# Performance work log

Measured on AMD Instinct MI355X. Metric: run time of the kernel, lower is better.

## Reference

```python
import jax, jax.numpy as jnp
import numpy as np

EPS = 1e-5
TOP_K = 2


def _dwconv3x3(x, w):
    # depthwise 3x3, stride 1, padding 1 (SAME)
    return jax.lax.conv_general_dilated(
        x, w, window_strides=(1, 1), padding='SAME',
        feature_group_count=x.shape[1],
        dimension_numbers=('NCHW', 'OIHW', 'NCHW'))


def _bn(x, g, b, m, v):
    # inference-mode BatchNorm2d
    s = g / jnp.sqrt(v + EPS)
    return x * s[None, :, None, None] + (b - m * s)[None, :, None, None]


def setup_inputs() -> dict:
    key = jax.random.key(0)
    ks = jax.random.split(key, 26)
    Bsz, D, H = 16, 384, 32
    S, E, HID = 64, 8, 768
    n, u = jax.random.normal, jax.random.uniform
    inp = {}
    inp['x'] = n(ks[0], (Bsz, D, H, H), jnp.float32)
    inp['dw1_w'] = n(ks[1], (D, 1, 3, 3)) * 0.1
    inp['bn1_g'] = u(ks[2], (D,), minval=0.5, maxval=1.5)
    inp['bn1_b'] = n(ks[3], (D,)) * 0.1
    inp['bn1_m'] = n(ks[4], (D,)) * 0.1
    inp['bn1_v'] = u(ks[5], (D,), minval=0.5, maxval=1.5)
    inp['dw2_w'] = n(ks[6], (D, 1, 3, 3)) * 0.1
    inp['bn2_g'] = u(ks[7], (D,), minval=0.5, maxval=1.5)
    inp['bn2_b'] = n(ks[8], (D,)) * 0.1
    inp['bn2_m'] = n(ks[9], (D,)) * 0.1
    inp['bn2_v'] = u(ks[10], (D,), minval=0.5, maxval=1.5)
    inp['ln_w'] = u(ks[11], (D,), minval=0.5, maxval=1.5)
    inp['ln_b'] = n(ks[12], (D,)) * 0.1
    inp['bcdt_w'] = n(ks[13], (3 * S, D)) * 0.02
    inp['dws_w'] = n(ks[14], (3 * S, 1, 3, 3)) * 0.1
    inp['hproj_w'] = n(ks[15], (D, D)) * 0.02
    inp['A'] = u(ks[16], (S,), minval=1.0, maxval=16.0)
    inp['gate_w'] = n(ks[17], (E, D)) * 0.02
    inp['gate_b'] = n(ks[18], (E,)) * 0.02
    inp['w1'] = n(ks[19], (E, HID, D)) * 0.02
    inp['b1'] = n(ks[20], (E, HID)) * 0.02
    inp['w2'] = n(ks[21], (E, D, HID)) * 0.02
    inp['b2'] = n(ks[22], (E, D)) * 0.02
    inp['w3'] = n(ks[23], (E, HID, D)) * 0.02
    inp['b3'] = n(ks[24], (E, HID)) * 0.02
    return inp


def reference(x, dw1_w, bn1_g, bn1_b, bn1_m, bn1_v, dw2_w, bn2_g, bn2_b, bn2_m,
              bn2_v, ln_w, ln_b, bcdt_w, dws_w, hproj_w, A, gate_w, gate_b,
              w1, b1, w2, b2, w3, b3):
    Bsz, D, H, W = x.shape
    L = H * W
    S = A.shape[0]
    E = gate_w.shape[0]
    # x = x + dwconv1(x)
    x = x + _bn(_dwconv3x3(x, dw1_w), bn1_g, bn1_b, bn1_m, bn1_v)
    x_prev = x
    # LayerNorm1D over channel dim of (B, C, L)
    xf = x.reshape(Bsz, D, L)
    mu = xf.mean(axis=1, keepdims=True)
    var = xf.var(axis=1, keepdims=True)
    xn = (xf - mu) / jnp.sqrt(var + EPS) * ln_w[None, :, None] + ln_b[None, :, None]
    # Slim_SSD mixer
    bcdt = jnp.einsum('cd,bdl->bcl', bcdt_w, xn)            # 1x1 conv1d
    bcdt = _dwconv3x3(bcdt.reshape(Bsz, 3 * S, H, W), dws_w).reshape(Bsz, 3 * S, L)
    Bm, Cm, dt = jnp.split(bcdt, 3, axis=1)                  # each (B, S, L)
    Am = jax.nn.softmax(dt + A[None, :, None], axis=-1)      # softmax over L
    h = jnp.einsum('bdl,bsl->bds', xn, Am * Bm)              # (B, D, S)
    h = jax.nn.silu(jnp.einsum('ed,bds->bes', hproj_w, h))   # h_proj + SiLU
    y = jnp.einsum('bes,bsl->bel', h, Cm).reshape(Bsz, D, H, W)
    x = x_prev + y
    # x = x + dwconv2(x)
    x = x + _bn(_dwconv3x3(x, dw2_w), bn2_g, bn2_b, bn2_m, bn2_v)
    # SparseMoE (TopkRouter, eval mode, filter_radio=0 -> mask==1, bias buffer==0)
    t = x.transpose(0, 2, 3, 1).reshape(-1, D)               # (N, D) tokens
    N = t.shape[0]
    logits = t @ gate_w.T + gate_b                           # (N, E)
    vals, idx = jax.lax.top_k(logits, TOP_K)
    probs = jax.nn.softmax(vals, axis=1)                     # softmax over top-k logits
    wfull = jnp.zeros((N, E), t.dtype).at[jnp.arange(N)[:, None], idx].set(probs)
    ymoe = jnp.zeros_like(t)
    for e in range(E):
        he = jax.nn.silu(t @ w1[e].T + b1[e]) * (t @ w3[e].T + b3[e])
        ymoe = ymoe + (he @ w2[e].T + b2[e]) * wfull[:, e:e + 1]
    x = x + ymoe.reshape(Bsz, H, W, D).transpose(0, 3, 1, 2)
    # dropout is identity in eval mode
    return (x, h)
```

## Files before the change

### kernel.cpp

```cpp
#include <hip/hip_runtime.h>
#include <hip/hip_bf16.h>

#define BSZ 16
#define DCH 384
#define LSP 1024
#define SST 64
#define NEXP 8
#define HID 768
#define NTOK 16384
#define MOE_MAXT 520

#define OFF_X1    0ULL
#define OFF_XN    25165824ULL
#define OFF_BCDT  50331648ULL
#define OFF_BCDTC 62914560ULL
#define OFF_H     75497472ULL
#define OFF_X2    77070336ULL
#define OFF_META  102236160ULL
#define OFF_LOGITS (OFF_META)
#define OFF_PROBS  (OFF_META +  524288ULL)
#define OFF_IDX    (OFF_META +  655360ULL)
#define OFF_CNT    (OFF_META +  786432ULL)
#define OFF_FILL   (OFF_META +  786464ULL)
#define OFF_OFFS   (OFF_META +  786496ULL)
#define OFF_TOFF   (OFF_META +  786560ULL)
#define OFF_LTOK   (OFF_META +  786624ULL)
#define OFF_LP     (OFF_META +  917696ULL)
#define OFF_TPOS   (OFF_META + 1048768ULL)
#define OFF_WBC    (OFF_META + 1179840ULL)
#define OFF_HE    0ULL
#define OFF_T16   OFF_BCDT
#define OFF_W1B   OFF_BCDTC
#define OFF_W3B   (OFF_BCDTC + 4718592ULL)
#define OFF_W2B   (OFF_BCDTC + 9437184ULL)
#define OFF_YMOE  OFF_X2
#define OFF_HPRE  OFF_X2
#define OFF_XNT   OFF_X2

typedef __attribute__((ext_vector_type(8))) short bf16x8;
typedef __attribute__((ext_vector_type(4))) float f32x4;
typedef __attribute__((ext_vector_type(4))) unsigned short u16x4;

__device__ __forceinline__ unsigned short f2bf(float f) {
  union { float f; unsigned int u; } x; x.f = f;
  unsigned int r = (x.u + 0x7fffu + ((x.u >> 16) & 1u)) >> 16;
  return (unsigned short)r;
}
__device__ __forceinline__ float bf2f(unsigned short s) {
  union { unsigned int u; float f; } x; x.u = ((unsigned int)s) << 16; return x.f;
}

__device__ __forceinline__ void async16(const void* g, void* l) {
  unsigned long long gi = reinterpret_cast<unsigned long long>(g);
  unsigned int li = (unsigned int)reinterpret_cast<unsigned long long>(l);
  __builtin_amdgcn_global_load_lds(
      (const __attribute__((address_space(1))) unsigned int*)gi,
      (__attribute__((address_space(3))) unsigned int*)(unsigned long long)li,
      16, 0, 0);
}

__global__ void k_dwbnres(const float* __restrict__ x, const float* __restrict__ w,
                          const float* __restrict__ g, const float* __restrict__ bb,
                          const float* __restrict__ mm, const float* __restrict__ vv,
                          float* __restrict__ out, int C) {
  int bc = blockIdx.x;
  int c = bc % C;
  __shared__ float tile[34 * 34];
  const float* img = x + (size_t)bc * 1024;
  for (int i = threadIdx.x; i < 34 * 34; i += 256) tile[i] = 0.f;
  __syncthreads();
  for (int i = threadIdx.x; i < 1024; i += 256) {
    int r = i >> 5, cc = i & 31;
    tile[(r + 1) * 34 + (cc + 1)] = img[i];
  }
  __syncthreads();
  float w0 = w[c*9+0], w1 = w[c*9+1], w2 = w[c*9+2], w3 = w[c*9+3], w4 = w[c*9+4],
        w5 = w[c*9+5], w6 = w[c*9+6], w7 = w[c*9+7], w8 = w[c*9+8];
  bool res = (g != nullptr);
  float scale = 1.f, bias = 0.f;
  if (res) { float s = g[c] * rsqrtf(vv[c] + 1e-5f); scale = s; bias = bb[c] - mm[c] * s; }
  for (int i = threadIdx.x; i < 1024; i += 256) {
    int r = i >> 5, cc = i & 31;
    const float* t0 = &tile[r * 34 + cc];
    float acc = t0[0]*w0 + t0[1]*w1 + t0[2]*w2
              + t0[34]*w3 + t0[35]*w4 + t0[36]*w5
              + t0[68]*w6 + t0[69]*w7 + t0[70]*w8;
    float o = res ? (t0[35] + acc * scale + bias) : acc;
    out[(size_t)bc * 1024 + i] = o;
  }
}

__global__ void k_layernorm(const float* __restrict__ x, const float* __restrict__ lw,
                            const float* __restrict__ lb, float* __restrict__ xn) {
  int lane = threadIdx.x & 63;
  int slice = threadIdx.x >> 6;
  int pos0 = blockIdx.x * 64;
  int b = pos0 >> 10;
  int l = (pos0 & 1023) + lane;
  const float* xb = x + (size_t)b * DCH * LSP + l;
  float s = 0.f, s2 = 0.f;
  for (int d = slice * 96; d < slice * 96 + 96; d++) {
    float v = xb[(size_t)d * LSP];
    s += v; s2 += v * v;
  }
  __shared__ float red[2][4][64];
  red[0][slice][lane] = s; red[1][slice][lane] = s2;
  __syncthreads();
  if (slice == 0) {
    s  = red[0][0][lane] + red[0][1][lane] + red[0][2][lane] + red[0][3][lane];
    s2 = red[1][0][lane] + red[1][1][lane] + red[1][2][lane] + red[1][3][lane];
    float mu = s * (1.f / 384.f);
    float var = s2 * (1.f / 384.f) - mu * mu;
    red[0][0][lane] = mu;
    red[1][0][lane] = rsqrtf(var + 1e-5f);
  }
  __syncthreads();
  float mu = red[0][0][lane], rs = red[1][0][lane];
  float* xnb = xn + (size_t)b * DCH * LSP + l;
  for (int d = slice * 96; d < slice * 96 + 96; d++) {
    float v = xb[(size_t)d * LSP];
    xnb[(size_t)d * LSP] = (v - mu) * rs * lw[d] + lb[d];
  }
}

__global__ void __launch_bounds__(256) k_bcdt(
    const unsigned short* __restrict__ xnT, const unsigned short* __restrict__ wbc,
    float* __restrict__ out) {
  int lt = blockIdx.x, ct = blockIdx.y, b = blockIdx.z;
  __shared__ unsigned short As[64 * 64];
  __shared__ unsigned short Bs[128 * 64];
  int tid = threadIdx.x;
  int lane = tid & 63, wave = tid >> 6;
  int wm = (wave & 1) * 32, wn = (wave >> 1) * 64;
  int fm = lane & 15, fq = lane >> 4;
  int srow = lane >> 3, slot = lane & 7;
  f32x4 acc[2][4];
  #pragma unroll
  for (int mi = 0; mi < 2; mi++)
    #pragma unroll
    for (int ni = 0; ni < 4; ni++) acc[mi][ni] = (f32x4)(0.f);
  const unsigned short* wge = wbc + (size_t)(ct * 64) * 384;
  const unsigned short* xge = xnT + ((size_t)(b * 1024 + lt * 128)) * 384;
  int ar0 = wave * 16 + srow, ar1 = ar0 + 8;
  const unsigned short* ag0 = wge + (size_t)ar0 * 384 + ((slot ^ (ar0 & 7)) * 8);
  const unsigned short* ag1 = wge + (size_t)ar1 * 384 + ((slot ^ (ar1 & 7)) * 8);
  const unsigned short* bg[4];
  #pragma unroll
  for (int ii = 0; ii < 4; ii++) {
    int brow = wave * 32 + ii * 8 + srow;
    bg[ii] = xge + (size_t)brow * 384 + ((slot ^ (brow & 7)) * 8);
  }
  unsigned short* asw0 = &As[(wave * 16) * 64];
  unsigned short* asw1 = &As[(wave * 16 + 8) * 64];
  for (int k0 = 0; k0 < 384; k0 += 64) {
    async16(ag0 + k0, asw0);
    async16(ag1 + k0, asw1);
    #pragma unroll
    for (int ii = 0; ii < 4; ii++)
      async16(bg[ii] + k0, &Bs[(wave * 32 + ii * 8) * 64]);
    __syncthreads();
    #pragma unroll
    for (int kk = 0; kk < 2; kk++) {
      int c = kk * 4 + fq;
      bf16x8 av[2];
      #pragma unroll
      for (int mi = 0; mi < 2; mi++) {
        int row = wm + mi * 16 + fm;
        av[mi] = *(bf16x8*)&As[row * 64 + ((c ^ (row & 7)) * 8)];
      }
      #pragma unroll
      for (int ni = 0; ni < 4; ni++) {
        int row = wn + ni * 16 + fm;
        bf16x8 bv = *(bf16x8*)&Bs[row * 64 + ((c ^ (row & 7)) * 8)];
        #pragma unroll
        for (int mi = 0; mi < 2; mi++)
          acc[mi][ni] = __builtin_amdgcn_mfma_f32_16x16x32_bf16(av[mi], bv, acc[mi][ni], 0, 0, 0);
      }
    }
    __syncthreads();
  }
  float* ob = out + (size_t)b * 196608 + (size_t)(ct * 64) * 1024 + lt * 128;
  #pragma unroll
  for (int mi = 0; mi < 2; mi++)
    #pragma unroll
    for (int ni = 0; ni < 4; ni++)
      #pragma unroll
      for (int r = 0; r < 4; r++) {
        int row = wm + mi * 16 + fq * 4 + r;
        int col = wn + ni * 16 + fm;
        ob[(size_t)row * 1024 + col] = acc[mi][ni][r];
      }
}

__global__ void k_softmax(float* __restrict__ bc, const float* __restrict__ Av) {
  int b = blockIdx.x >> 6, s = blockIdx.x & 63;
  float* row = bc + (size_t)b * 196608 + (size_t)(128 + s) * 1024;
  float a = Av[s];
  int t = threadIdx.x;
  float v[4]; float mx = -3.0e38f;
  #pragma unroll
  for (int i = 0; i < 4; i++) { v[i] = row[t + 256 * i] + a; mx = fmaxf(mx, v[i]); }
  #pragma unroll
  for (int off = 32; off >= 1; off >>= 1) mx = fmaxf(mx, __shfl_xor(mx, off));
  __shared__ float redm[4], reds[4];
  if ((t & 63) == 0) redm[t >> 6] = mx;
  __syncthreads();
  mx = fmaxf(fmaxf(redm[0], redm[1]), fmaxf(redm[2], redm[3]));
  float sm = 0.f;
  #pragma unroll
  for (int i = 0; i < 4; i++) { v[i] = __expf(v[i] - mx); sm += v[i]; }
  #pragma unroll
  for (int off = 32; off >= 1; off >>= 1) sm += __shfl_xor(sm, off);
  if ((t & 63) == 0) reds[t >> 6] = sm;
  __syncthreads();
  sm = reds[0] + reds[1] + reds[2] + reds[3];
  float inv = 1.f / sm;
  #pragma unroll
  for (int i = 0; i < 4; i++) row[t + 256 * i] = v[i] * inv;
}

__global__ void k_h(const float* __restrict__ xn, const float* __restrict__ bc,
                    float* __restrict__ h) {
  int dt_ = blockIdx.x, ls = blockIdx.y, b = blockIdx.z;
  __shared__ float xs[64][65];
  __shared__ float ab[64][65];
  int tid = threadIdx.x;
  int sg4 = tid & 15, dg4 = tid >> 4;
  float acc[4][4];
  #pragma unroll
  for (int i = 0; i < 4; i++)
    #pragma unroll
    for (int j = 0; j < 4; j++) acc[i][j] = 0.f;
  const float* Bm = bc + (size_t)b * 196608;
  const float* Am = Bm + 131072;
  const float* xb = xn + (size_t)b * DCH * LSP + (size_t)(dt_ * 64) * LSP;
  for (int l0 = ls * 128; l0 < ls * 128 + 128; l0 += 64) {
    for (int i = tid; i < 4096; i += 256) {
      int r = i >> 6, ll = i & 63;
      xs[r][ll] = xb[(size_t)r * LSP + l0 + ll];
      ab[r][ll] = Am[(size_t)r * 1024 + l0 + ll] * Bm[(size_t)r * 1024 + l0 + ll];
    }
    __syncthreads();
    for (int ll = 0; ll < 64; ll++) {
      float xv[4], av[4];
      #pragma unroll
      for (int i = 0; i < 4; i++) xv[i] = xs[dg4 * 4 + i][ll];
      #pragma unroll
      for (int j = 0; j < 4; j++) av[j] = ab[sg4 * 4 + j][ll];
      #pragma unroll
      for (int i = 0; i < 4; i++)
        #pragma unroll
        for (int j = 0; j < 4; j++) acc[i][j] += xv[i] * av[j];
    }
    __syncthreads();
  }
  float* hb = h + (size_t)b * DCH * SST + (size_t)(dt_ * 64) * 64;
  #pragma unroll
  for (int i = 0; i < 4; i++)
    #pragma unroll
    for (int j = 0; j < 4; j++)
      atomicAdd(&hb[(size_t)(dg4 * 4 + i) * 64 + sg4 * 4 + j], acc[i][j]);
}

__global__ void k_hproj(const float* __restrict__ h, const float* __restrict__ pw,
                        float* __restrict__ hpre) {
  int et = blockIdx.x, ks = blockIdx.y, b = blockIdx.z;
  __shared__ float hs[64][65];
  __shared__ float ps[64][65];
  int tid = threadIdx.x;
  int sg4 = tid & 15, eg4 = tid >> 4;
  float acc[4][4];
  #pragma unroll
  for (int i = 0; i < 4; i++)
    #pragma unroll
    for (int j = 0; j < 4; j++) acc[i][j] = 0.f;
  for (int d0 = ks * 128; d0 < ks * 128 + 128; d0 += 64) {
    for (int i = tid; i < 4096; i += 256) {
      int r = i >> 6, cc = i & 63;
      hs[r][cc] = h[(size_t)b * DCH * SST + (size_t)(d0 + r) * 64 + cc];
      ps[r][cc] = pw[(size_t)(et * 64 + r) * 384 + d0 + cc];
    }
    __syncthreads();
    for (int dd = 0; dd < 64; dd++) {
      float pv[4], hv[4];
      #pragma unroll
      for (int i = 0; i < 4; i++) pv[i] = ps[eg4 * 4 + i][dd];
      #pragma unroll
      for (int j = 0; j < 4; j++) hv[j] = hs[dd][sg4 * 4 + j];
      #pragma unroll
      for (int i = 0; i < 4; i++)
        #pragma unroll
        for (int j = 0; j < 4; j++) acc[i][j] += pv[i] * hv[j];
    }
    __syncthreads();
  }
  float* hb = hpre + (size_t)b * DCH * SST + (size_t)(et * 64) * 64;
  #pragma unroll
  for (int i = 0; i < 4; i++)
    #pragma unroll
    for (int j = 0; j < 4; j++)
      atomicAdd(&hb[(size_t)(eg4 * 4 + i) * 64 + sg4 * 4 + j], acc[i][j]);
}

__global__ void k_silu(const float* __restrict__ hpre, float* __restrict__ h2) {
  int i = blockIdx.x * 256 + threadIdx.x;
  float4 v = ((const float4*)hpre)[i];
  v.x = v.x / (1.f + __expf(-v.x));
  v.y = v.y / (1.f + __expf(-v.y));
  v.z = v.z / (1.f + __expf(-v.z));
  v.w = v.w / (1.f + __expf(-v.w));
  ((float4*)h2)[i] = v;
}

__global__ void k_y(const float* __restrict__ h2, const float* __restrict__ bc,
                    const float* __restrict__ x1, float* __restrict__ x2) {
  int lt = blockIdx.x, dt_ = blockIdx.y, b = blockIdx.z;
  __shared__ float hss[32][65];
  __shared__ float cs[64][129];
  int lg = threadIdx.x & 31, dg = threadIdx.x >> 5;
  float acc[4][4];
  for (int i = 0; i < 4; i++) for (int j = 0; j < 4; j++) acc[i][j] = 0.f;
  for (int i = threadIdx.x; i < 2048; i += 256) {
    int r = i >> 6, cc = i & 63;
    hss[r][cc] = h2[(size_t)b * DCH * SST + (size_t)(dt_ * 32 + r) * 64 + cc];
  }
  const float* Cm = bc + (size_t)b * 196608 + 65536;
  for (int i = threadIdx.x; i < 8192; i += 256) {
    int ss = i >> 7, ll = i & 127;
    cs[ss][ll] = Cm[(size_t)ss * 1024 + lt * 128 + ll];
  }
  __syncthreads();
  for (int ss = 0; ss < 64; ss++) {
    float cv[4];
    #pragma unroll
    for (int il = 0; il < 4; il++) cv[il] = cs[ss][lg + 32 * il];
    #pragma unroll
    for (int id = 0; id < 4; id++) {
      float hv = hss[dg * 4 + id][ss];
      #pragma unroll
      for (int il = 0; il < 4; il++) acc[id][il] += hv * cv[il];
    }
  }
  size_t base = (size_t)b * DCH * LSP + (size_t)(dt_ * 32) * LSP + lt * 128;
  for (int id = 0; id < 4; id++)
    for (int il = 0; il < 4; il++) {
      size_t o = base + (size_t)(dg * 4 + id) * LSP + lg + 32 * il;
      x2[o] = x1[o] + acc[id][il];
    }
}

__global__ void k_router(const float* __restrict__ x3, const float* __restrict__ gw,
                         const float* __restrict__ gb, float* __restrict__ logits) {
  __shared__ float xs[64][65];
  __shared__ float gs[8][64];
  int blk = blockIdx.x;
  int b = blk >> 4; int l0 = (blk & 15) * 64;
  int lg = threadIdx.x & 63, eg = threadIdx.x >> 6;
  float acc0 = 0.f, acc1 = 0.f;
  const float* xb = x3 + (size_t)b * DCH * LSP + l0;
  for (int d0 = 0; d0 < 384; d0 += 64) {
    for (int i = threadIdx.x; i < 4096; i += 256) {
      int dd = i >> 6, ll = i & 63;
      xs[dd][ll] = xb[(size_t)(d0 + dd) * LSP + ll];
    }
    for (int i = threadIdx.x; i < 512; i += 256) {
      int e = i >> 6, dd = i & 63;
      gs[e][dd] = gw[(size_t)e * 384 + d0 + dd];
    }
    __syncthreads();
    for (int dd = 0; dd < 64; dd++) {
      float xv = xs[dd][lg];
      acc0 += gs[eg][dd] * xv;
      acc1 += gs[eg + 4][dd] * xv;
    }
    __syncthreads();
  }
  int n = b * 1024 + l0 + lg;
  logits[(size_t)n * 8 + eg]     = acc0 + gb[eg];
  logits[(size_t)n * 8 + eg + 4] = acc1 + gb[eg + 4];
}

__global__ void k_topk(const float* __restrict__ logits, float* __restrict__ probs,
                       int* __restrict__ idx, int* __restrict__ cnt) {
  __shared__ int lcnt[8];
  if (threadIdx.x < 8) lcnt[threadIdx.x] = 0;
  __syncthreads();
  int n = blockIdx.x * 256 + threadIdx.x;
  float lv[8];
  for (int e = 0; e < 8; e++) lv[e] = logits[(size_t)n * 8 + e];
  int i1 = 0; float v1 = lv[0];
  for (int e = 1; e < 8; e++) if (lv[e] > v1) { v1 = lv[e]; i1 = e; }
  int i2 = -1; float v2 = -3.0e38f;
  for (int e = 0; e < 8; e++) { if (e == i1) continue; if (lv[e] > v2) { v2 = lv[e]; i2 = e; } }
  float p1 = 1.f / (1.f + __expf(v2 - v1));
  probs[n * 2] = p1; probs[n * 2 + 1] = 1.f - p1;
  idx[n * 2] = i1; idx[n * 2 + 1] = i2;
  atomicAdd(&lcnt[i1], 1); atomicAdd(&lcnt[i2], 1);
  __syncthreads();
  if (threadIdx.x < 8) atomicAdd(&cnt[threadIdx.x], lcnt[threadIdx.x]);
}

__global__ void k_offsets(const int* __restrict__ cnt, int* __restrict__ offs,
                          int* __restrict__ toff) {
  if (threadIdx.x == 0) {
    int a = 0, t = 0;
    for (int e = 0; e < 8; e++) {
      offs[e] = a; toff[e] = t;
      a += cnt[e]; t += (cnt[e] + 63) >> 6;
    }
    toff[8] = t;
  }
}

__global__ void k_build(const int* __restrict__ idx, const float* __restrict__ probs,
                        const int* __restrict__ offs, int* __restrict__ fill,
                        int* __restrict__ ltok, float* __restrict__ lp,
                        int* __restrict__ tpos) {
  __shared__ int lcnt[8], lbase[8];
  if (threadIdx.x < 8) lcnt[threadIdx.x] = 0;
  __syncthreads();
  int n = blockIdx.x * 256 + threadIdx.x;
  int e0 = idx[n * 2], e1 = idx[n * 2 + 1];
  int o0 = atomicAdd(&lcnt[e0], 1);
  int o1 = atomicAdd(&lcnt[e1], 1);
  __syncthreads();
  if (threadIdx.x < 8) lbase[threadIdx.x] = atomicAdd(&fill[threadIdx.x], lcnt[threadIdx.x]);
  __syncthreads();
  int p0 = offs[e0] + lbase[e0] + o0;
  int p1 = offs[e1] + lbase[e1] + o1;
  ltok[p0] = n; lp[p0] = probs[n * 2];     tpos[n * 2] = p0;
  ltok[p1] = n; lp[p1] = probs[n * 2 + 1]; tpos[n * 2 + 1] = p1;
}

__global__ void k_t16(const float* __restrict__ x3, unsigned short* __restrict__ t16) {
  __shared__ float tl[32][33];
  int lt = blockIdx.x, dt_ = blockIdx.y, b = blockIdx.z;
  const float* xb = x3 + (size_t)b * DCH * LSP + (size_t)(dt_ * 32) * LSP + lt * 32;
  for (int i = threadIdx.x; i < 1024; i += 256) {
    int dd = i >> 5, ll = i & 31;
    tl[dd][ll] = xb[(size_t)dd * LSP + ll];
  }
  __syncthreads();
  for (int i = threadIdx.x; i < 1024; i += 256) {
    int ll = i >> 5, dd = i & 31;
    int n = b * 1024 + lt * 32 + ll;
    t16[(size_t)n * 384 + dt_ * 32 + dd] = f2bf(tl[dd][ll]);
  }
}

__global__ void k_wbf(const float* __restrict__ s, unsigned short* __restrict__ d) {
  int i = blockIdx.x * 256 + threadIdx.x;
  float4 v = ((const float4*)s)[i];
  u16x4 o;
  o.x = f2bf(v.x); o.y = f2bf(v.y); o.z = f2bf(v.z); o.w = f2bf(v.w);
  ((u16x4*)d)[i] = o;
}

__global__ void k_f2bf3(const float* __restrict__ s0, const float* __restrict__ s1,
                        const float* __restrict__ s2, unsigned short* __restrict__ d0,
                        unsigned short* __restrict__ d1, unsigned short* __restrict__ d2,
                        int n4) {
  int i = blockIdx.x * 256 + threadIdx.x;
  if (i >= n4) return;
  const float* s = (blockIdx.y == 0) ? s0 : (blockIdx.y == 1) ? s1 : s2;
  unsigned short* d = (blockIdx.y == 0) ? d0 : (blockIdx.y == 1) ? d1 : d2;
  float4 v = ((const float4*)s)[i];
  u16x4 o;
  o.x = f2bf(v.x); o.y = f2bf(v.y); o.z = f2bf(v.z); o.w = f2bf(v.w);
  ((u16x4*)d)[i] = o;
}

__global__ void __launch_bounds__(256) k_moe1(
    const unsigned short* __restrict__ t16, const unsigned short* __restrict__ w1,
    const unsigned short* __restrict__ w3, const float* __restrict__ b1,
    const float* __restrict__ b3, const int* __restrict__ ltok,
    const int* __restrict__ cnt, const int* __restrict__ offs,
    const int* __restrict__ toff, unsigned short* __restrict__ he) {
  int tb = blockIdx.x;
  if (tb >= toff[8]) return;
  int e = 0;
  #pragma unroll
  for (int i = 1; i < 8; i++) if (toff[i] <= tb) e = i;
  int rt = tb - toff[e];
  int ne = cnt[e], base = offs[e];
  int ct = blockIdx.y;
  __shared__ unsigned short As[64 * 64];
  __shared__ unsigned short B1s[128 * 64];
  __shared__ unsigned short B3s[128 * 64];
  __shared__ int toks[64];
  int tid = threadIdx.x;
  if (tid < 64) {
    int r = rt * 64 + tid;
    toks[tid] = ltok[base + (r < ne ? r : ne - 1)];
  }
  __syncthreads();
  int lane = tid & 63, wave = tid >> 6;
  int wm = (wave & 1) * 32, wn = (wave >> 1) * 64;
  int fm = lane & 15, fq = lane >> 4;
  int srow = lane >> 3, slot = lane & 7;
  f32x4 acc1[2][4], acc3[2][4];
  #pragma unroll
  for (int mi = 0; mi < 2; mi++)
    #pragma unroll
    for (int ni = 0; ni < 4; ni++) { acc1[mi][ni] = (f32x4)(0.f); acc3[mi][ni] = (f32x4)(0.f); }
  const unsigned short* w1e = w1 + ((size_t)e * 768 + ct * 128) * 384;
  const unsigned short* w3e = w3 + ((size_t)e * 768 + ct * 128) * 384;
  int ar0 = wave * 16 + srow, ar1 = wave * 16 + 8 + srow;
  const unsigned short* ag0 = t16 + (size_t)toks[ar0] * 384 + ((slot ^ (ar0 & 7)) * 8);
  const unsigned short* ag1 = t16 + (size_t)toks[ar1] * 384 + ((slot ^ (ar1 & 7)) * 8);
  const unsigned short* b1g[4]; const unsigned short* b3g[4];
  #pragma unroll
  for (int ii = 0; ii < 4; ii++) {
    int brow = wave * 32 + ii * 8 + srow;
    int coff = (slot ^ (brow & 7)) * 8;
    b1g[ii] = w1e + (size_t)brow * 384 + coff;
    b3g[ii] = w3e + (size_t)brow * 384 + coff;
  }
  unsigned short* asw0 = &As[(wave * 16) * 64];
  unsigned short* asw1 = &As[(wave * 16 + 8) * 64];
  for (int k0 = 0; k0 < 384; k0 += 64) {
    async16(ag0 + k0, asw0);
    async16(ag1 + k0, asw1);
    #pragma unroll
    for (int ii = 0; ii < 4; ii++) {
      async16(b1g[ii] + k0, &B1s[(wave * 32 + ii * 8) * 64]);
      async16(b3g[ii] + k0, &B3s[(wave * 32 + ii * 8) * 64]);
    }
    __syncthreads();
    #pragma unroll
    for (int kk = 0; kk < 2; kk++) {
      int c = kk * 4 + fq;
      bf16x8 av[2];
      #pragma unroll
      for (int mi = 0; mi < 2; mi++) {
        int row = wm + mi * 16 + fm;
        av[mi] = *(bf16x8*)&As[row * 64 + ((c ^ (row & 7)) * 8)];
      }
      #pragma unroll
      for (int ni = 0; ni < 4; ni++) {
        int row = wn + ni * 16 + fm;
        int off = row * 64 + ((c ^ (row & 7)) * 8);
        bf16x8 b1v = *(bf16x8*)&B1s[off];
        bf16x8 b3v = *(bf16x8*)&B3s[off];
        #pragma unroll
        for (int mi = 0; mi < 2; mi++) {
          acc1[mi][ni] = __builtin_amdgcn_mfma_f32_16x16x32_bf16(av[mi], b1v, acc1[mi][ni], 0, 0, 0);
          acc3[mi][ni] = __builtin_amdgcn_mfma_f32_16x16x32_bf16(av[mi], b3v, acc3[mi][ni], 0, 0, 0);
        }
      }
    }
    __syncthreads();
  }
  #pragma unroll
  for (int mi = 0; mi < 2; mi++)
    #pragma unroll
    for (int ni = 0; ni < 4; ni++)
      #pragma unroll
      for (int r = 0; r < 4; r++) {
        int lr = wm + mi * 16 + fq * 4 + r;
        int gr = rt * 64 + lr;
        if (gr < ne) {
          int col = ct * 128 + wn + ni * 16 + fm;
          float z1 = acc1[mi][ni][r] + b1[e * 768 + col];
          float z3 = acc3[mi][ni][r] + b3[e * 768 + col];
          float val = (z1 / (1.f + __expf(-z1))) * z3;
          he[((size_t)base + gr) * 768 + col] = f2bf(val);
        }
      }
}

__global__ void __launch_bounds__(256) k_moe2(
    const unsigned short* __restrict__ he, const unsigned short* __restrict__ w2,
    const float* __restrict__ b2, const float* __restrict__ lp,
    const int* __restrict__ cnt, const int* __restrict__ offs,
    const int* __restrict__ toff, unsigned short* __restrict__ ymoe) {
  int tb = blockIdx.x;
  if (tb >= toff[8]) return;
  int e = 0;
  #pragma unroll
  for (int i = 1; i < 8; i++) if (toff[i] <= tb) e = i;
  int rt = tb - toff[e];
  int ne = cnt[e], base = offs[e];
  int ct = blockIdx.y;
  __shared__ unsigned short As[64 * 64];
  __shared__ unsigned short Bs[128 * 64];
  __shared__ float lps[64];
  int tid = threadIdx.x;
  if (tid < 64) {
    int r = rt * 64 + tid;
    lps[tid] = lp[base + (r < ne ? r : ne - 1)];
  }
  int lane = tid & 63, wave = tid >> 6;
  int wm = (wave & 1) * 32, wn = (wave >> 1) * 64;
  int fm = lane & 15, fq = lane >> 4;
  int srow = lane >> 3, slot = lane & 7;
  f32x4 acc[2][4];
  #pragma unroll
  for (int mi = 0; mi < 2; mi++)
    #pragma unroll
    for (int ni = 0; ni < 4; ni++) acc[mi][ni] = (f32x4)(0.f);
  const unsigned short* w2e = w2 + ((size_t)e * 384 + ct * 128) * 768;
  int ar0 = wave * 16 + srow, ar1 = wave * 16 + 8 + srow;
  int g0 = base + rt * 64 + ar0; if (g0 > 32767) g0 = 32767;
  int g1 = base + rt * 64 + ar1; if (g1 > 32767) g1 = 32767;
  const unsigned short* ag0 = he + (size_t)g0 * 768 + ((slot ^ (ar0 & 7)) * 8);
  const unsigned short* ag1 = he + (size_t)g1 * 768 + ((slot ^ (ar1 & 7)) * 8);
  const unsigned short* bg[4];
  #pragma unroll
  for (int ii = 0; ii < 4; ii++) {
    int brow = wave * 32 + ii * 8 + srow;
    bg[ii] = w2e + (size_t)brow * 768 + ((slot ^ (brow & 7)) * 8);
  }
  unsigned short* asw0 = &As[(wave * 16) * 64];
  unsigned short* asw1 = &As[(wave * 16 + 8) * 64];
  for (int k0 = 0; k0 < 768; k0 += 64) {
    async16(ag0 + k0, asw0);
    async16(ag1 + k0, asw1);
    #pragma unroll
    for (int ii = 0; ii < 4; ii++)
      async16(bg[ii] + k0, &Bs[(wave * 32 + ii * 8) * 64]);
    __syncthreads();
    #pragma unroll
    for (int kk = 0; kk < 2; kk++) {
      int c = kk * 4 + fq;
      bf16x8 av[2];
      #pragma unroll
      for (int mi = 0; mi < 2; mi++) {
        int row = wm + mi * 16 + fm;
        av[mi] = *(bf16x8*)&As[row * 64 + ((c ^ (row & 7)) * 8)];
      }
      #pragma unroll
      for (int ni = 0; ni < 4; ni++) {
        int row = wn + ni * 16 + fm;
        bf16x8 bv = *(bf16x8*)&Bs[row * 64 + ((c ^ (row & 7)) * 8)];
        #pragma unroll
        for (int mi = 0; mi < 2; mi++)
          acc[mi][ni] = __builtin_amdgcn_mfma_f32_16x16x32_bf16(av[mi], bv, acc[mi][ni], 0, 0, 0);
      }
    }
    __syncthreads();
  }
  #pragma unroll
  for (int mi = 0; mi < 2; mi++)
    #pragma unroll
    for (int ni = 0; ni < 4; ni++)
      #pragma unroll
      for (int r = 0; r < 4; r++) {
        int lr = wm + mi * 16 + fq * 4 + r;
        int gr = rt * 64 + lr;
        if (gr < ne) {
          int col = ct * 128 + wn + ni * 16 + fm;
          float val = (acc[mi][ni][r] + b2[e * 384 + col]) * lps[lr];
          ymoe[((size_t)base + gr) * 384 + col] = f2bf(val);
        }
      }
}

__global__ void k_scatter(const unsigned short* __restrict__ ymoe,
                          const int* __restrict__ tpos, float* __restrict__ xout) {
  int dt_ = blockIdx.x;
  int lt = blockIdx.y;
  int b = blockIdx.z;
  int l = threadIdx.x & 63;
  int d0 = dt_ * 32 + (threadIdx.x >> 6) * 8;
  int n = b * 1024 + lt * 64 + l;
  int p0 = tpos[2 * n], p1 = tpos[2 * n + 1];
  bf16x8 y0 = *(const bf16x8*)(ymoe + (size_t)p0 * 384 + d0);
  bf16x8 y1 = *(const bf16x8*)(ymoe + (size_t)p1 * 384 + d0);
  size_t base = (size_t)b * DCH * LSP + (size_t)d0 * LSP + lt * 64 + l;
  #pragma unroll
  for (int k = 0; k < 8; k++) {
    float v = bf2f((unsigned short)y0[k]) + bf2f((unsigned short)y1[k]);
    xout[base + (size_t)k * LSP] += v;
  }
}

extern "C" void kernel_launch(void* const* d_in, const int* in_sizes, int n_in,
                              void* d_out, int out_size, void* d_ws, size_t ws_size,
                              hipStream_t stream) {
  const float* x      = (const float*)d_in[0];
  const float* dw1    = (const float*)d_in[1];
  const float* bn1g   = (const float*)d_in[2];
  const float* bn1b   = (const float*)d_in[3];
  const float* bn1m   = (const float*)d_in[4];
  const float* bn1v   = (const float*)d_in[5];
  const float* dw2    = (const float*)d_in[6];
  const float* bn2g   = (const float*)d_in[7];
  const float* bn2b   = (const float*)d_in[8];
  const float* bn2m   = (const float*)d_in[9];
  const float* bn2v   = (const float*)d_in[10];
  const float* lnw    = (const float*)d_in[11];
  const float* lnb    = (const float*)d_in[12];
  const float* bcdtw  = (const float*)d_in[13];
  const float* dwsw   = (const float*)d_in[14];
  const float* hprojw = (const float*)d_in[15];
  const float* Avec   = (const float*)d_in[16];
  const float* gatew  = (const float*)d_in[17];
  const float* gateb  = (const float*)d_in[18];
  const float* w1f    = (const float*)d_in[19];
  const float* b1f    = (const float*)d_in[20];
  const float* w2f    = (const float*)d_in[21];
  const float* b2f    = (const float*)d_in[22];
  const float* w3f    = (const float*)d_in[23];
  const float* b3f    = (const float*)d_in[24];

  char* wsb = (char*)d_ws;
  float* x1    = (float*)(wsb + OFF_X1);
  float* xn    = (float*)(wsb + OFF_XN);
  float* bcdt  = (float*)(wsb + OFF_BCDT);
  float* bcdtc = (float*)(wsb + OFF_BCDTC);
  float* hbuf  = (float*)(wsb + OFF_H);
  float* hpre  = (float*)(wsb + OFF_HPRE);
  float* x2    = (float*)(wsb + OFF_X2);
  float* logits = (float*)(wsb + OFF_LOGITS);
  float* probs  = (float*)(wsb + OFF_PROBS);
  int*   idx    = (int*)(wsb + OFF_IDX);
  int*   cnt    = (int*)(wsb + OFF_CNT);
  int*   fill   = (int*)(wsb + OFF_FILL);
  int*   offs   = (int*)(wsb + OFF_OFFS);
  int*   toff   = (int*)(wsb + OFF_TOFF);
  int*   ltok   = (int*)(wsb + OFF_LTOK);
  float* lp     = (float*)(wsb + OFF_LP);
  int*   tpos   = (int*)(wsb + OFF_TPOS);
  unsigned short* t16  = (unsigned short*)(wsb + OFF_T16);
  unsigned short* w1b  = (unsigned short*)(wsb + OFF_W1B);
  unsigned short* w3b  = (unsigned short*)(wsb + OFF_W3B);
  unsigned short* w2b  = (unsigned short*)(wsb + OFF_W2B);
  unsigned short* he   = (unsigned short*)(wsb + OFF_HE);
  unsigned short* ymoe = (unsigned short*)(wsb + OFF_YMOE);
  unsigned short* xnT  = (unsigned short*)(wsb + OFF_XNT);
  unsigned short* wbc  = (unsigned short*)(wsb + OFF_WBC);
  float* xout = (float*)d_out;
  float* h2   = xout + (size_t)BSZ * DCH * LSP;

  k_dwbnres<<<BSZ * DCH, 256, 0, stream>>>(x, dw1, bn1g, bn1b, bn1m, bn1v, x1, DCH);
  k_layernorm<<<NTOK / 64, 256, 0, stream>>>(x1, lnw, lnb, xn);
  k_t16<<<dim3(32, 12, BSZ), 256, 0, stream>>>(xn, xnT);
  k_wbf<<<72, 256, 0, stream>>>(bcdtw, wbc);
  k_bcdt<<<dim3(8, 3, BSZ), 256, 0, stream>>>(xnT, wbc, bcdt);
  k_dwbnres<<<BSZ * 192, 256, 0, stream>>>(bcdt, dwsw, nullptr, nullptr, nullptr, nullptr, bcdtc, 192);
  k_softmax<<<BSZ * SST, 256, 0, stream>>>(bcdtc, Avec);
  hipMemsetAsync(hbuf, 0, (size_t)BSZ * DCH * SST * 4, stream);
  hipMemsetAsync(hpre, 0, (size_t)BSZ * DCH * SST * 4, stream);
  k_h<<<dim3(6, 8, BSZ), 256, 0, stream>>>(xn, bcdtc, hbuf);
  k_hproj<<<dim3(6, 3, BSZ), 256, 0, stream>>>(hbuf, hprojw, hpre);
  k_silu<<<(BSZ * DCH * SST / 4) / 256, 256, 0, stream>>>(hpre, h2);
  k_y<<<dim3(8, 12, BSZ), 256, 0, stream>>>(h2, bcdtc, x1, x2);
  k_dwbnres<<<BSZ * DCH, 256, 0, stream>>>(x2, dw2, bn2g, bn2b, bn2m, bn2v, xout, DCH);
  hipMemsetAsync(wsb + OFF_CNT, 0, 64, stream);
  k_router<<<256, 256, 0, stream>>>(xout, gatew, gateb, logits);
  k_topk<<<NTOK / 256, 256, 0, stream>>>(logits, probs, idx, cnt);
  k_offsets<<<1, 64, 0, stream>>>(cnt, offs, toff);
  k_build<<<NTOK / 256, 256, 0, stream>>>(idx, probs, offs, fill, ltok, lp, tpos);
  k_t16<<<dim3(32, 12, BSZ), 256, 0, stream>>>(xout, t16);
  int n4 = NEXP * HID * DCH / 4;
  k_f2bf3<<<dim3((n4 + 255) / 256, 3), 256, 0, stream>>>(w1f, w3f, w2f, w1b, w3b, w2b, n4);
  k_moe1<<<dim3(MOE_MAXT, 6), 256, 0, stream>>>(t16, w1b, w3b, b1f, b3f, ltok, cnt, offs, toff, he);
  k_moe2<<<dim3(MOE_MAXT, 3), 256, 0, stream>>>(he, w2b, b2f, lp, cnt, offs, toff, ymoe);
  k_scatter<<<dim3(12, 16, BSZ), 256, 0, stream>>>(ymoe, tpos, xout);
}
```

Before: 505.6 us.

## Enlarge MoE GEMM row tiles to 128 tokens and swap grid axes

```diff
diff --git a/kernel.cpp b/kernel.cpp
--- a/kernel.cpp
+++ b/kernel.cpp
@@ -8,7 +8,7 @@
 #define NEXP 8
 #define HID 768
 #define NTOK 16384
-#define MOE_MAXT 520
+#define MOE_MAXT 264
 
 #define OFF_X1    0ULL
 #define OFF_XN    25165824ULL
@@ -406,7 +406,7 @@
     int a = 0, t = 0;
     for (int e = 0; e < 8; e++) {
       offs[e] = a; toff[e] = t;
-      a += cnt[e]; t += (cnt[e] + 63) >> 6;
+      a += cnt[e]; t += (cnt[e] + 127) >> 7;
     }
     toff[8] = t;
   }
@@ -470,80 +470,76 @@
   ((u16x4*)d)[i] = o;
 }
 
-__global__ void __launch_bounds__(256) k_moe1(
+__global__ void __launch_bounds__(256, 2) k_moe1(
     const unsigned short* __restrict__ t16, const unsigned short* __restrict__ w1,
     const unsigned short* __restrict__ w3, const float* __restrict__ b1,
     const float* __restrict__ b3, const int* __restrict__ ltok,
     const int* __restrict__ cnt, const int* __restrict__ offs,
     const int* __restrict__ toff, unsigned short* __restrict__ he) {
-  int tb = blockIdx.x;
+  int tb = blockIdx.y;
   if (tb >= toff[8]) return;
   int e = 0;
   #pragma unroll
   for (int i = 1; i < 8; i++) if (toff[i] <= tb) e = i;
   int rt = tb - toff[e];
   int ne = cnt[e], base = offs[e];
-  int ct = blockIdx.y;
-  __shared__ unsigned short As[64 * 64];
+  int ct = blockIdx.x;
+  __shared__ unsigned short As[128 * 64];
   __shared__ unsigned short B1s[128 * 64];
   __shared__ unsigned short B3s[128 * 64];
-  __shared__ int toks[64];
+  __shared__ int toks[128];
   int tid = threadIdx.x;
-  if (tid < 64) {
-    int r = rt * 64 + tid;
+  if (tid < 128) {
+    int r = rt * 128 + tid;
     toks[tid] = ltok[base + (r < ne ? r : ne - 1)];
   }
   __syncthreads();
   int lane = tid & 63, wave = tid >> 6;
-  int wm = (wave & 1) * 32, wn = (wave >> 1) * 64;
+  int rh = wave & 1, ch = wave >> 1;
   int fm = lane & 15, fq = lane >> 4;
   int srow = lane >> 3, slot = lane & 7;
-  f32x4 acc1[2][4], acc3[2][4];
-  #pragma unroll
-  for (int mi = 0; mi < 2; mi++)
+  f32x4 acc1[4][4], acc3[4][4];
+  #pragma unroll
+  for (int mi = 0; mi < 4; mi++)
     #pragma unroll
     for (int ni = 0; ni < 4; ni++) { acc1[mi][ni] = (f32x4)(0.f); acc3[mi][ni] = (f32x4)(0.f); }
   const unsigned short* w1e = w1 + ((size_t)e * 768 + ct * 128) * 384;
   const unsigned short* w3e = w3 + ((size_t)e * 768 + ct * 128) * 384;
-  int ar0 = wave * 16 + srow, ar1 = wave * 16 + 8 + srow;
-  const unsigned short* ag0 = t16 + (size_t)toks[ar0] * 384 + ((slot ^ (ar0 & 7)) * 8);
-  const unsigned short* ag1 = t16 + (size_t)toks[ar1] * 384 + ((slot ^ (ar1 & 7)) * 8);
-  const unsigned short* b1g[4]; const unsigned short* b3g[4];
+  const unsigned short* ag[4]; const unsigned short* b1g[4]; const unsigned short* b3g[4];
   #pragma unroll
   for (int ii = 0; ii < 4; ii++) {
-    int brow = wave * 32 + ii * 8 + srow;
-    int coff = (slot ^ (brow & 7)) * 8;
-    b1g[ii] = w1e + (size_t)brow * 384 + coff;
-    b3g[ii] = w3e + (size_t)brow * 384 + coff;
-  }
-  unsigned short* asw0 = &As[(wave * 16) * 64];
-  unsigned short* asw1 = &As[(wave * 16 + 8) * 64];
+    int row = wave * 32 + ii * 8 + srow;
+    int coff = (slot ^ (row & 7)) * 8;
+    ag[ii]  = t16 + (size_t)toks[row] * 384 + coff;
+    b1g[ii] = w1e + (size_t)row * 384 + coff;
+    b3g[ii] = w3e + (size_t)row * 384 + coff;
+  }
   for (int k0 = 0; k0 < 384; k0 += 64) {
-    async16(ag0 + k0, asw0);
-    async16(ag1 + k0, asw1);
     #pragma unroll
     for (int ii = 0; ii < 4; ii++) {
-      async16(b1g[ii] + k0, &B1s[(wave * 32 + ii * 8) * 64]);
-      async16(b3g[ii] + k0, &B3s[(wave * 32 + ii * 8) * 64]);
+      unsigned int lb = (wave * 32 + ii * 8) * 64;
+      async16(ag[ii]  + k0, &As[lb]);
+      async16(b1g[ii] + k0, &B1s[lb]);
+      async16(b3g[ii] + k0, &B3s[lb]);
     }
     __syncthreads();
     #pragma unroll
     for (int kk = 0; kk < 2; kk++) {
       int c = kk * 4 + fq;
-      bf16x8 av[2];
-      #pragma unroll
-      for (int mi = 0; mi < 2; mi++) {
-        int row = wm + mi * 16 + fm;
+      bf16x8 av[4];
+      #pragma unroll
+      for (int mi = 0; mi < 4; mi++) {
+        int row = rh * 64 + mi * 16 + fm;
         av[mi] = *(bf16x8*)&As[row * 64 + ((c ^ (row & 7)) * 8)];
       }
       #pragma unroll
       for (int ni = 0; ni < 4; ni++) {
-        int row = wn + ni * 16 + fm;
+        int row = ch * 64 + ni * 16 + fm;
         int off = row * 64 + ((c ^ (row & 7)) * 8);
         bf16x8 b1v = *(bf16x8*)&B1s[off];
         bf16x8 b3v = *(bf16x8*)&B3s[off];
         #pragma unroll
-        for (int mi = 0; mi < 2; mi++) {
+        for (int mi = 0; mi < 4; mi++) {
           acc1[mi][ni] = __builtin_amdgcn_mfma_f32_16x16x32_bf16(av[mi], b1v, acc1[mi][ni], 0, 0, 0);
           acc3[mi][ni] = __builtin_amdgcn_mfma_f32_16x16x32_bf16(av[mi], b3v, acc3[mi][ni], 0, 0, 0);
         }
@@ -552,15 +548,15 @@
     __syncthreads();
   }
   #pragma unroll
-  for (int mi = 0; mi < 2; mi++)
+  for (int mi = 0; mi < 4; mi++)
     #pragma unroll
     for (int ni = 0; ni < 4; ni++)
       #pragma unroll
       for (int r = 0; r < 4; r++) {
-        int lr = wm + mi * 16 + fq * 4 + r;
-        int gr = rt * 64 + lr;
+        int lr = rh * 64 + mi * 16 + fq * 4 + r;
+        int gr = rt * 128 + lr;
         if (gr < ne) {
-          int col = ct * 128 + wn + ni * 16 + fm;
+          int col = ct * 128 + ch * 64 + ni * 16 + fm;
           float z1 = acc1[mi][ni][r] + b1[e * 768 + col];
           float z3 = acc3[mi][ni][r] + b3[e * 768 + col];
           float val = (z1 / (1.f + __expf(-z1))) * z3;
@@ -569,87 +565,84 @@
       }
 }
 
-__global__ void __launch_bounds__(256) k_moe2(
+__global__ void __launch_bounds__(256, 3) k_moe2(
     const unsigned short* __restrict__ he, const unsigned short* __restrict__ w2,
     const float* __restrict__ b2, const float* __restrict__ lp,
     const int* __restrict__ cnt, const int* __restrict__ offs,
     const int* __restrict__ toff, unsigned short* __restrict__ ymoe) {
-  int tb = blockIdx.x;
+  int tb = blockIdx.y;
   if (tb >= toff[8]) return;
   int e = 0;
   #pragma unroll
   for (int i = 1; i < 8; i++) if (toff[i] <= tb) e = i;
   int rt = tb - toff[e];
   int ne = cnt[e], base = offs[e];
-  int ct = blockIdx.y;
-  __shared__ unsigned short As[64 * 64];
+  int ct = blockIdx.x;
+  __shared__ unsigned short As[128 * 64];
   __shared__ unsigned short Bs[128 * 64];
-  __shared__ float lps[64];
+  __shared__ float lps[128];
   int tid = threadIdx.x;
-  if (tid < 64) {
-    int r = rt * 64 + tid;
+  if (tid < 128) {
+    int r = rt * 128 + tid;
     lps[tid] = lp[base + (r < ne ? r : ne - 1)];
   }
   int lane = tid & 63, wave = tid >> 6;
-  int wm = (wave & 1) * 32, wn = (wave >> 1) * 64;
+  int rh = wave & 1, ch = wave >> 1;
   int fm = lane & 15, fq = lane >> 4;
   int srow = lane >> 3, slot = lane & 7;
-  f32x4 acc[2][4];
-  #pragma unroll
-  for (int mi = 0; mi < 2; mi++)
+  f32x4 acc[4][4];
+  #pragma unroll
+  for (int mi = 0; mi < 4; mi++)
     #pragma unroll
     for (int ni = 0; ni < 4; ni++) acc[mi][ni] = (f32x4)(0.f);
   const unsigned short* w2e = w2 + ((size_t)e * 384 + ct * 128) * 768;
-  int ar0 = wave * 16 + srow, ar1 = wave * 16 + 8 + srow;
-  int g0 = base + rt * 64 + ar0; if (g0 > 32767) g0 = 32767;
-  int g1 = base + rt * 64 + ar1; if (g1 > 32767) g1 = 32767;
-  const unsigned short* ag0 = he + (size_t)g0 * 768 + ((slot ^ (ar0 & 7)) * 8);
-  const unsigned short* ag1 = he + (size_t)g1 * 768 + ((slot ^ (ar1 & 7)) * 8);
-  const unsigned short* bg[4];
+  const unsigned short* ag[4]; const unsigned short* bg[4];
   #pragma unroll
   for (int ii = 0; ii < 4; ii++) {
-    int brow = wave * 32 + ii * 8 + srow;
-    bg[ii] = w2e + (size_t)brow * 768 + ((slot ^ (brow & 7)) * 8);
-  }
-  unsigned short* asw0 = &As[(wave * 16) * 64];
-  unsigned short* asw1 = &As[(wave * 16 + 8) * 64];
+    int row = wave * 32 + ii * 8 + srow;
+    int coff = (slot ^ (row & 7)) * 8;
+    int g = base + rt * 128 + row; if (g > 32767) g = 32767;
+    ag[ii] = he + (size_t)g * 768 + coff;
+    bg[ii] = w2e + (size_t)row * 768 + coff;
+  }
   for (int k0 = 0; k0 < 768; k0 += 64) {
-    async16(ag0 + k0, asw0);
-    async16(ag1 + k0, asw1);
-    #pragma unroll
-    for (int ii = 0; ii < 4; ii++)
-      async16(bg[ii] + k0, &Bs[(wave * 32 + ii * 8) * 64]);
+    #pragma unroll
+    for (int ii = 0; ii < 4; ii++) {
+      unsigned int lb = (wave * 32 + ii * 8) * 64;
+      async16(ag[ii] + k0, &As[lb]);
+      async16(bg[ii] + k0, &Bs[lb]);
+    }
     __syncthreads();
     #pragma unroll
     for (int kk = 0; kk < 2; kk++) {
       int c = kk * 4 + fq;
-      bf16x8 av[2];
-      #pragma unroll
-      for (int mi = 0; mi < 2; mi++) {
-        int row = wm + mi * 16 + fm;
+      bf16x8 av[4];
+      #pragma unroll
+      for (int mi = 0; mi < 4; mi++) {
+        int row = rh * 64 + mi * 16 + fm;
         av[mi] = *(bf16x8*)&As[row * 64 + ((c ^ (row & 7)) * 8)];
       }
       #pragma unroll
       for (int ni = 0; ni < 4; ni++) {
-        int row = wn + ni * 16 + fm;
+        int row = ch * 64 + ni * 16 + fm;
         bf16x8 bv = *(bf16x8*)&Bs[row * 64 + ((c ^ (row & 7)) * 8)];
         #pragma unroll
-        for (int mi = 0; mi < 2; mi++)
+        for (int mi = 0; mi < 4; mi++)
           acc[mi][ni] = __builtin_amdgcn_mfma_f32_16x16x32_bf16(av[mi], bv, acc[mi][ni], 0, 0, 0);
       }
     }
     __syncthreads();
   }
   #pragma unroll
-  for (int mi = 0; mi < 2; mi++)
+  for (int mi = 0; mi < 4; mi++)
     #pragma unroll
     for (int ni = 0; ni < 4; ni++)
       #pragma unroll
       for (int r = 0; r < 4; r++) {
-        int lr = wm + mi * 16 + fq * 4 + r;
-        int gr = rt * 64 + lr;
+        int lr = rh * 64 + mi * 16 + fq * 4 + r;
+        int gr = rt * 128 + lr;
         if (gr < ne) {
-          int col = ct * 128 + wn + ni * 16 + fm;
+          int col = ct * 128 + ch * 64 + ni * 16 + fm;
           float val = (acc[mi][ni][r] + b2[e * 384 + col]) * lps[lr];
           ymoe[((size_t)base + gr) * 384 + col] = f2bf(val);
         }
@@ -755,7 +748,7 @@
   k_t16<<<dim3(32, 12, BSZ), 256, 0, stream>>>(xout, t16);
   int n4 = NEXP * HID * DCH / 4;
   k_f2bf3<<<dim3((n4 + 255) / 256, 3), 256, 0, stream>>>(w1f, w3f, w2f, w1b, w3b, w2b, n4);
-  k_moe1<<<dim3(MOE_MAXT, 6), 256, 0, stream>>>(t16, w1b, w3b, b1f, b3f, ltok, cnt, offs, toff, he);
-  k_moe2<<<dim3(MOE_MAXT, 3), 256, 0, stream>>>(he, w2b, b2f, lp, cnt, offs, toff, ymoe);
+  k_moe1<<<dim3(6, MOE_MAXT), 256, 0, stream>>>(t16, w1b, w3b, b1f, b3f, ltok, cnt, offs, toff, he);
+  k_moe2<<<dim3(3, MOE_MAXT), 256, 0, stream>>>(he, w2b, b2f, lp, cnt, offs, toff, ymoe);
   k_scatter<<<dim3(12, 16, BSZ), 256, 0, stream>>>(ymoe, tpos, xout);
 }
```

After: 532.6 us. 5.3% more time.
